# Performance work log

Measured on AMD Instinct MI355X. Metric: run time of the kernel, lower is better.

## Reference

```python
import jax, jax.numpy as jnp
import numpy as np

B, T, C = 4, 2048, 1024
H = 16                      # n_head
D = C // H                  # head dim = 64
FF = 4 * C                  # 4096


def setup_inputs() -> dict:
    key = jax.random.key(0)
    ks = jax.random.split(key, 9)
    s = 0.02
    return {
        "x": jax.random.normal(ks[0], (B, T, C), dtype=jnp.float32),
        # LayerNorm params (elementwise affine, default torch init)
        "ln1_w": jnp.ones((C,), jnp.float32),
        "ln1_b": jnp.zeros((C,), jnp.float32),
        "ln2_w": jnp.ones((C,), jnp.float32),
        "ln2_b": jnp.zeros((C,), jnp.float32),
        # attention weights, torch Linear layout [out, in], bias=False
        "w_attn": jax.random.normal(ks[1], (3 * C, C), jnp.float32) * s,
        "w_proj": jax.random.normal(ks[2], (C, C), jnp.float32) * s,
        # FFN weights
        "w_fc": jax.random.normal(ks[3], (FF, C), jnp.float32) * s,
        "w_fc_proj": jax.random.normal(ks[4], (C, FF), jnp.float32) * s,
    }


def _layernorm(x, w, b, eps=1e-5):
    mu = jnp.mean(x, axis=-1, keepdims=True)
    var = jnp.var(x, axis=-1, keepdims=True)
    return (x - mu) * jax.lax.rsqrt(var + eps) * w + b


def _attn(h, w_attn, w_proj):
    qkv = jnp.einsum('btc,fc->btf', h, w_attn)        # [B,T,3C]
    q, k, v = jnp.split(qkv, 3, axis=-1)
    q = q.reshape(B, T, H, D).transpose(0, 2, 1, 3)   # [B,H,T,D]
    k = k.reshape(B, T, H, D).transpose(0, 2, 1, 3)
    v = v.reshape(B, T, H, D).transpose(0, 2, 1, 3)
    att = jnp.einsum('bhtd,bhsd->bhts', q, k) * (1.0 / np.sqrt(D))
    causal = jnp.tril(jnp.ones((T, T), dtype=bool))
    att = jnp.where(causal, att, -jnp.inf)
    att = jax.nn.softmax(att, axis=-1)
    y = jnp.einsum('bhts,bhsd->bhtd', att, v)         # [B,H,T,D]
    y = y.transpose(0, 2, 1, 3).reshape(B, T, C)
    return jnp.einsum('btc,oc->bto', y, w_proj)


def _ffn(h, w_fc, w_fc_proj):
    u = jax.nn.gelu(jnp.einsum('btc,fc->btf', h, w_fc), approximate=False)
    return jnp.einsum('btf,cf->btc', u, w_fc_proj)


def reference(x, ln1_w, ln1_b, ln2_w, ln2_b, w_attn, w_proj, w_fc, w_fc_proj):
    x = x + _attn(_layernorm(x, ln1_w, ln1_b), w_attn, w_proj)
    x = x + _ffn(_layernorm(x, ln2_w, ln2_b), w_fc, w_fc_proj)
    return x
```

## Files before the change

kernel.cpp:

```cpp
#include <hip/hip_runtime.h>
#include <hip/hip_bf16.h>

using bf16 = __hip_bfloat16;
typedef __attribute__((ext_vector_type(8))) short short8;
typedef __attribute__((ext_vector_type(4))) short sh4;
typedef __attribute__((ext_vector_type(4))) float f32x4;

#define B_ 4
#define T_ 2048
#define C_ 1024
#define H_ 16
#define FF_ 4096
#define M_TOK (B_ * T_)

#define BARRIER() asm volatile("s_barrier" ::: "memory")
#define WAITLGKM0() asm volatile("s_waitcnt lgkmcnt(0)" ::: "memory")
#define WAITLGKM8() asm volatile("s_waitcnt lgkmcnt(8)" ::: "memory")
#define WAITVM4() asm volatile("s_waitcnt vmcnt(4)" ::: "memory")
#define WAITVM2() asm volatile("s_waitcnt vmcnt(2)" ::: "memory")
#define WAITVM0() asm volatile("s_waitcnt vmcnt(0)" ::: "memory")

__device__ __forceinline__ void gload16(const void* g, void* l) {
    __builtin_amdgcn_global_load_lds(
        (const __attribute__((address_space(1))) void*)g,
        (__attribute__((address_space(3))) void*)l, 16, 0, 0);
}

__device__ __forceinline__ float fexp2(float x) {
    float r;
    asm("v_exp_f32 %0, %1" : "=v"(r) : "v"(x));
    return r;
}

__device__ __forceinline__ float bf16bits2f(short s) {
    return __uint_as_float(((unsigned)(unsigned short)s) << 16);
}

template <int CTRL>
__device__ __forceinline__ float dpp_rotf(float x) {
    return __int_as_float(__builtin_amdgcn_update_dpp(
        0, __float_as_int(x), CTRL, 0xf, 0xf, true));
}
__device__ __forceinline__ float red16_max(float v) {
    v = fmaxf(v, dpp_rotf<0x128>(v));
    v = fmaxf(v, dpp_rotf<0x124>(v));
    v = fmaxf(v, dpp_rotf<0x122>(v));
    v = fmaxf(v, dpp_rotf<0x121>(v));
    return v;
}
__device__ __forceinline__ float red16_sum(float v) {
    v += dpp_rotf<0x128>(v);
    v += dpp_rotf<0x124>(v);
    v += dpp_rotf<0x122>(v);
    v += dpp_rotf<0x121>(v);
    return v;
}

__global__ void cvt_f32_bf16_v4(const float* __restrict__ in, bf16* __restrict__ out, int n4) {
    int i = blockIdx.x * blockDim.x + threadIdx.x;
    if (i < n4) {
        float4 v = ((const float4*)in)[i];
        sh4 o;
        bf16 b0 = __float2bfloat16(v.x), b1 = __float2bfloat16(v.y),
             b2 = __float2bfloat16(v.z), b3 = __float2bfloat16(v.w);
        o[0] = *(short*)&b0; o[1] = *(short*)&b1;
        o[2] = *(short*)&b2; o[3] = *(short*)&b3;
        ((sh4*)out)[i] = o;
    }
}

template <typename TIN>
__global__ __launch_bounds__(256) void ln_kernel(const TIN* __restrict__ x,
                                                 const float* __restrict__ w,
                                                 const float* __restrict__ b,
                                                 bf16* __restrict__ out) {
    int row = blockIdx.x;
    int t = threadIdx.x;
    float4 v;
    if constexpr (sizeof(TIN) == 4) {
        v = ((const float4*)(x + (size_t)row * C_))[t];
    } else {
        sh4 h = ((const sh4*)(x + (size_t)row * C_))[t];
        v.x = bf16bits2f(h[0]);
        v.y = bf16bits2f(h[1]);
        v.z = bf16bits2f(h[2]);
        v.w = bf16bits2f(h[3]);
    }
    float s = v.x + v.y + v.z + v.w;
    float s2 = v.x * v.x + v.y * v.y + v.z * v.z + v.w * v.w;
#pragma unroll
    for (int off = 32; off > 0; off >>= 1) {
        s += __shfl_down(s, off);
        s2 += __shfl_down(s2, off);
    }
    __shared__ float ss[4], ss2[4];
    int wave = t >> 6, lane = t & 63;
    if (lane == 0) { ss[wave] = s; ss2[wave] = s2; }
    __syncthreads();
    s = ss[0] + ss[1] + ss[2] + ss[3];
    s2 = ss2[0] + ss2[1] + ss2[2] + ss2[3];
    float mu = s * (1.f / C_);
    float var = s2 * (1.f / C_) - mu * mu;
    float rstd = rsqrtf(var + 1e-5f);
    float4 wv = ((const float4*)w)[t];
    float4 bv = ((const float4*)b)[t];
    sh4 o;
    bf16 b0 = __float2bfloat16((v.x - mu) * rstd * wv.x + bv.x);
    bf16 b1 = __float2bfloat16((v.y - mu) * rstd * wv.y + bv.y);
    bf16 b2 = __float2bfloat16((v.z - mu) * rstd * wv.z + bv.z);
    bf16 b3 = __float2bfloat16((v.w - mu) * rstd * wv.w + bv.w);
    o[0] = *(short*)&b0; o[1] = *(short*)&b1;
    o[2] = *(short*)&b2; o[3] = *(short*)&b3;
    ((sh4*)(out + (size_t)row * C_))[t] = o;
}

#define STG(ldsbase, g, grow0, k0)                                               \
    {                                                                            \
        _Pragma("unroll") for (int s_ = 0; s_ < 2; s_++) {                       \
            int row_ = s_ * 64 + wid * 8 + sr;                                   \
            gload16(g + (size_t)((grow0) + row_) * K + (k0) + ssc,               \
                    (ldsbase) + row_ * 64 + (lane & 7) * 8);                     \
        }                                                                        \
    }

#define HALF256 (128 * 64)
template <int EPI>
__global__ __launch_bounds__(512, 2) void gemm256(const bf16* __restrict__ Ag,
                                                  const bf16* __restrict__ Bg,
                                                  void* __restrict__ Cout,
                                                  int M, int N, int K) {
    __shared__ short SA[2][256 * 64];
    __shared__ short SB[2][256 * 64];

    const int nbx = N >> 8;
    const int nwg = nbx * (M >> 8);
    const int bid = blockIdx.x;
    const int cpx = nwg >> 3;
    const int swzb = (bid & 7) * cpx + (bid >> 3);
    const int m0 = (swzb / nbx) * 256;
    const int n0 = (swzb % nbx) * 256;

    const int t = threadIdx.x;
    const int wid = t >> 6, lane = t & 63;
    const int wm = wid >> 2, wn = wid & 3;
    const int lrow = lane & 15, lg = lane >> 4;
    const int swzr = (lane & 7) * 8;
    const int sr = lane >> 3;
    const int ssc = ((lane & 7) ^ sr) * 8;

    f32x4 acc[8][4];
#pragma unroll
    for (int mi = 0; mi < 8; mi++)
#pragma unroll
        for (int ni = 0; ni < 4; ni++) acc[mi][ni] = (f32x4){0.f, 0.f, 0.f, 0.f};
    short8 bfr[4][2];

    const int T = K >> 6;
    const int niter = T >> 1;

#define DSREADS256(q, buf)                                                       \
    if ((q) == 0) {                                                              \
        _Pragma("unroll") for (int ni = 0; ni < 4; ni++)                         \
        _Pragma("unroll") for (int ks = 0; ks < 2; ks++)                         \
            bfr[ni][ks] = *(const short8*)(&SB[buf][(wn * 64 + ni * 16 + lrow) * 64 + \
                                                    ((ks * 32 + lg * 8) ^ swzr)]);    \
    }                                                                            \
    _Pragma("unroll") for (int mi2 = 0; mi2 < 2; mi2++)                          \
    _Pragma("unroll") for (int ks = 0; ks < 2; ks++)                             \
        af[mi2 * 2 + ks] = *(const short8*)(&SA[buf][(wm * 128 + (2 * (q) + mi2) * 16 + lrow) * 64 + \
                                                     ((ks * 32 + lg * 8) ^ swzr)]);

#define MFMAS256(q)                                                              \
    __builtin_amdgcn_s_setprio(1);                                               \
    _Pragma("unroll") for (int ks = 0; ks < 2; ks++)                             \
    _Pragma("unroll") for (int ni = 0; ni < 4; ni++)                             \
    _Pragma("unroll") for (int mi2 = 0; mi2 < 2; mi2++)                          \
        acc[2 * (q) + mi2][ni] = __builtin_amdgcn_mfma_f32_16x16x32_bf16(        \
            af[mi2 * 2 + ks], bfr[ni][ks], acc[2 * (q) + mi2][ni], 0, 0, 0);     \
    __builtin_amdgcn_s_setprio(0);

    STG(&SA[0][0], Ag, m0, 0);
    STG(&SA[0][HALF256], Ag, m0 + 128, 0);
    STG(&SB[0][0], Bg, n0, 0);
    STG(&SB[0][HALF256], Bg, n0 + 128, 0);
    STG(&SB[1][0], Bg, n0, 64);
    STG(&SB[1][HALF256], Bg, n0 + 128, 64);
    WAITVM4();
    BARRIER();

    for (int iter = 0; iter < niter; iter++) {
        const int tt = 2 * iter;
        const int ka = (tt + 1) * 64, kb = (tt + 2) * 64, kc = (tt + 3) * 64;
        const bool s2 = (tt + 2 < T), s3 = (tt + 3 < T);
        const bool last = (iter == niter - 1);
        short8 af[4];

        DSREADS256(0, 0);
        STG(&SA[1][0], Ag, m0, ka);
        WAITLGKM8();
        BARRIER(); WAITLGKM0(); MFMAS256(0); BARRIER();
        DSREADS256(1, 0);
        STG(&SA[1][HALF256], Ag, m0 + 128, ka);
        BARRIER(); WAITLGKM0(); MFMAS256(1); BARRIER();
        DSREADS256(2, 0);
        if (s2) STG(&SB[0][0], Bg, n0, kb);
        BARRIER(); WAITLGKM0(); MFMAS256(2); BARRIER();
        DSREADS256(3, 0);
        if (s2) STG(&SB[0][HALF256], Bg, n0 + 128, kb);
        BARRIER(); WAITLGKM0(); MFMAS256(3);
        if (last) { WAITVM0(); } else { WAITVM4(); }
        BARRIER();
        DSREADS256(0, 1);
        if (s2) STG(&SA[0][0], Ag, m0, kb);
        WAITLGKM8();
        BARRIER(); WAITLGKM0(); MFMAS256(0); BARRIER();
        DSREADS256(1, 1);
        if (s2) STG(&SA[0][HALF256], Ag, m0 + 128, kb);
        BARRIER(); WAITLGKM0(); MFMAS256(1); BARRIER();
        DSREADS256(2, 1);
        if (s3) STG(&SB[1][0], Bg, n0, kc);
        BARRIER(); WAITLGKM0(); MFMAS256(2); BARRIER();
        DSREADS256(3, 1);
        if (s3) STG(&SB[1][HALF256], Bg, n0 + 128, kc);
        BARRIER(); WAITLGKM0(); MFMAS256(3);
        if (!last) WAITVM4();
        BARRIER();
    }

#pragma unroll
    for (int mi = 0; mi < 8; mi++) {
#pragma unroll
        for (int ni = 0; ni < 4; ni++) {
            int gr = m0 + wm * 128 + mi * 16 + lg * 4;
            int gc = n0 + wn * 64 + ni * 16 + lrow;
#pragma unroll
            for (int r = 0; r < 4; r++) {
                size_t gi = (size_t)(gr + r) * N + gc;
                float v = acc[mi][ni][r];
                if constexpr (EPI == 0) {
                    ((bf16*)Cout)[gi] = __float2bfloat16(v);
                } else {
                    float ge = 0.5f * v * (1.f + erff(v * 0.70710678f));
                    ((bf16*)Cout)[gi] = __float2bfloat16(ge);
                }
            }
        }
    }
}

template <int EPI>
__global__ __launch_bounds__(512, 2) void gemm256x128(const bf16* __restrict__ Ag,
                                                      const bf16* __restrict__ Bg,
                                                      void* __restrict__ Cout,
                                                      const void* __restrict__ Res,
                                                      int M, int N, int K) {
    __shared__ short SA[2][256 * 64];
    __shared__ short SB[2][128 * 64];

    const int nbx = N >> 7;
    const int nwg = nbx * (M >> 8);
    const int bid = blockIdx.x;
    const int cpx = nwg >> 3;
    const int swzb = (bid & 7) * cpx + (bid >> 3);
    const int m0 = (swzb / nbx) * 256;
    const int n0 = (swzb % nbx) * 128;

    const int t = threadIdx.x;
    const int wid = t >> 6, lane = t & 63;
    const int wm = wid >> 1, wn = wid & 1;
    const int lrow = lane & 15, lg = lane >> 4;
    const int swzr = (lane & 7) * 8;
    const int sr = lane >> 3;
    const int ssc = ((lane & 7) ^ sr) * 8;

    f32x4 acc[4][4];
#pragma unroll
    for (int mi = 0; mi < 4; mi++)
#pragma unroll
        for (int ni = 0; ni < 4; ni++) acc[mi][ni] = (f32x4){0.f, 0.f, 0.f, 0.f};
    short8 bfr[4][2];

    const int T = K >> 6;
    const int niter = T >> 1;

#define DSRX(p, buf)                                                             \
    if ((p) == 0) {                                                              \
        _Pragma("unroll") for (int ni = 0; ni < 4; ni++)                         \
        _Pragma("unroll") for (int ks = 0; ks < 2; ks++)                         \
            bfr[ni][ks] = *(const short8*)(&SB[buf][(wn * 64 + ni * 16 + lrow) * 64 + \
                                                    ((ks * 32 + lg * 8) ^ swzr)]);    \
    }                                                                            \
    _Pragma("unroll") for (int mi2 = 0; mi2 < 2; mi2++)                          \
    _Pragma("unroll") for (int ks = 0; ks < 2; ks++)                             \
        af[mi2 * 2 + ks] = *(const short8*)(&SA[buf][(wm * 64 + (2 * (p) + mi2) * 16 + lrow) * 64 + \
                                                     ((ks * 32 + lg * 8) ^ swzr)]);

#define MFX(p)                                                                   \
    __builtin_amdgcn_s_setprio(1);                                               \
    _Pragma("unroll") for (int ks = 0; ks < 2; ks++)                             \
    _Pragma("unroll") for (int ni = 0; ni < 4; ni++)                             \
    _Pragma("unroll") for (int mi2 = 0; mi2 < 2; mi2++)                          \
        acc[2 * (p) + mi2][ni] = __builtin_amdgcn_mfma_f32_16x16x32_bf16(        \
            af[mi2 * 2 + ks], bfr[ni][ks], acc[2 * (p) + mi2][ni], 0, 0, 0);     \
    __builtin_amdgcn_s_setprio(0);

    STG(&SA[0][0], Ag, m0, 0);
    STG(&SA[0][HALF256], Ag, m0 + 128, 0);
    STG(&SB[0][0], Bg, n0, 0);
    STG(&SB[1][0], Bg, n0, 64);
    WAITVM2();
    BARRIER();

    for (int iter = 0; iter < niter; iter++) {
        const int tt = 2 * iter;
        const int ka = (tt + 1) * 64, kb = (tt + 2) * 64, kc = (tt + 3) * 64;
        const bool s2 = (tt + 2 < T), s3 = (tt + 3 < T);
        const bool last = (iter == niter - 1);
        short8 af[4];

        DSRX(0, 0);
        STG(&SA[1][0], Ag, m0, ka);
        STG(&SA[1][HALF256], Ag, m0 + 128, ka);
        WAITLGKM8();
        BARRIER(); WAITLGKM0(); MFX(0); BARRIER();
        DSRX(1, 0);
        if (s2) STG(&SB[0][0], Bg, n0, kb);
        BARRIER(); WAITLGKM0(); MFX(1);
        if (last) { WAITVM0(); } else { WAITVM2(); }
        BARRIER();
        DSRX(0, 1);
        if (s2) {
            STG(&SA[0][0], Ag, m0, kb);
            STG(&SA[0][HALF256], Ag, m0 + 128, kb);
        }
        WAITLGKM8();
        BARRIER(); WAITLGKM0(); MFX(0); BARRIER();
        DSRX(1, 1);
        if (s3) STG(&SB[1][0], Bg, n0, kc);
        BARRIER(); WAITLGKM0(); MFX(1);
        if (last) { WAITVM0(); } else { WAITVM2(); }
        BARRIER();
    }

#pragma unroll
    for (int mi = 0; mi < 4; mi++) {
#pragma unroll
        for (int ni = 0; ni < 4; ni++) {
            int gr = m0 + wm * 64 + mi * 16 + lg * 4;
            int gc = n0 + wn * 64 + ni * 16 + lrow;
#pragma unroll
            for (int r = 0; r < 4; r++) {
                size_t gi = (size_t)(gr + r) * N + gc;
                float v = acc[mi][ni][r];
                if constexpr (EPI == 0) {
                    ((bf16*)Cout)[gi] = __float2bfloat16(v);
                } else if constexpr (EPI == 3) {
                    float res = ((const float*)Res)[gi];
                    ((bf16*)Cout)[gi] = __float2bfloat16(res + v);
                } else {
                    float res = __bfloat162float(((const bf16*)Res)[gi]);
                    ((float*)Cout)[gi] = res + v;
                }
            }
        }
    }
}

__global__ __launch_bounds__(256) void flash_attn(const bf16* __restrict__ qk,
                                                  const bf16* __restrict__ vt,
                                                  bf16* __restrict__ y) {
    const int pi = blockIdx.x;
    const int bh = blockIdx.y;
    const int b = bh >> 4, h = bh & 15;
    const int t = threadIdx.x;
    const int wave = t >> 6, lane = t & 63;
    const int lrow = lane & 15, g = lane >> 4, lk = g * 8;

    __shared__ alignas(16) short Ks[64 * 72];
    __shared__ alignas(16) short Vs[64 * 72];
    __shared__ alignas(16) short Ps[128 * 72];

    const size_t rs = 2 * C_;
    const bf16* Qg = qk + (size_t)b * T_ * rs + h * 64;
    const bf16* Kg = Qg + C_;
    const bf16* Vg = vt + (size_t)(h * 64) * M_TOK + b * T_;

    const int srow = t >> 3;
    const int sc8 = (t & 7) * 8;
    const float scale2 = 0.125f * 1.44269504089f;

    for (int sel = 0; sel < 2; sel++) {
        const int qtb = sel ? pi : 15 - pi;
        const int q0 = qtb * 128;
        const int nkt = 2 * qtb + 2;

        short8 qf[2][2];
#pragma unroll
        for (int mi = 0; mi < 2; mi++) {
            const bf16* qr = Qg + (size_t)(q0 + wave * 32 + mi * 16 + lrow) * rs;
            qf[mi][0] = *(const short8*)(qr + lk);
            qf[mi][1] = *(const short8*)(qr + 32 + lk);
        }

        f32x4 o[2][4];
        float m[2][4], l[2][4];
#pragma unroll
        for (int mi = 0; mi < 2; mi++) {
#pragma unroll
            for (int ni = 0; ni < 4; ni++) o[mi][ni] = (f32x4){0.f, 0.f, 0.f, 0.f};
#pragma unroll
            for (int r = 0; r < 4; r++) { m[mi][r] = -1e30f; l[mi][r] = 0.f; }
        }

        short8 kr[2], vr[2];
#pragma unroll
        for (int p = 0; p < 2; p++) {
            int r = srow + p * 32;
            kr[p] = *(const short8*)(Kg + (size_t)r * rs + sc8);
            vr[p] = *(const short8*)(Vg + (size_t)r * M_TOK + sc8);
        }

        for (int kt = 0; kt < nkt; kt++) {
            const int s0 = kt * 64;
#pragma unroll
            for (int p = 0; p < 2; p++) {
                int r = srow + p * 32;
                *(short8*)(&Ks[r * 72 + sc8]) = kr[p];
                *(short8*)(&Vs[r * 72 + sc8]) = vr[p];
            }
            __syncthreads();
            if (kt + 1 < nkt) {
                const int s0n = (kt + 1) * 64;
#pragma unroll
                for (int p = 0; p < 2; p++) {
                    int r = srow + p * 32;
                    kr[p] = *(const short8*)(Kg + (size_t)(s0n + r) * rs + sc8);
                    vr[p] = *(const short8*)(Vg + (size_t)r * M_TOK + s0n + sc8);
                }
            }

            f32x4 s[2][4];
#pragma unroll
            for (int mi = 0; mi < 2; mi++)
#pragma unroll
                for (int ni = 0; ni < 4; ni++) s[mi][ni] = (f32x4){0.f, 0.f, 0.f, 0.f};
            __builtin_amdgcn_s_setprio(1);
#pragma unroll
            for (int ks = 0; ks < 2; ks++) {
#pragma unroll
                for (int ni = 0; ni < 4; ni++) {
                    short8 kf = *(const short8*)(&Ks[(ni * 16 + lrow) * 72 + ks * 32 + lk]);
#pragma unroll
                    for (int mi = 0; mi < 2; mi++)
                        s[mi][ni] = __builtin_amdgcn_mfma_f32_16x16x32_bf16(
                            qf[mi][ks], kf, s[mi][ni], 0, 0, 0);
                }
            }
            __builtin_amdgcn_s_setprio(0);

            if (kt >= nkt - 2) {
#pragma unroll
                for (int mi = 0; mi < 2; mi++)
#pragma unroll
                    for (int ni = 0; ni < 4; ni++)
#pragma unroll
                        for (int r = 0; r < 4; r++) {
                            int qg = q0 + wave * 32 + mi * 16 + g * 4 + r;
                            int kvg = s0 + ni * 16 + lrow;
                            s[mi][ni][r] = (kvg > qg) ? -1e30f : s[mi][ni][r] * scale2;
                        }
            } else {
#pragma unroll
                for (int mi = 0; mi < 2; mi++)
#pragma unroll
                    for (int ni = 0; ni < 4; ni++)
#pragma unroll
                        for (int r = 0; r < 4; r++) s[mi][ni][r] *= scale2;
            }

#pragma unroll
            for (int mi = 0; mi < 2; mi++) {
                float pm[4];
#pragma unroll
                for (int r = 0; r < 4; r++) {
                    float v = fmaxf(fmaxf(s[mi][0][r], s[mi][1][r]),
                                    fmaxf(s[mi][2][r], s[mi][3][r]));
                    pm[r] = red16_max(v);
                }
                int ok = (pm[0] <= m[mi][0] + 8.f) && (pm[1] <= m[mi][1] + 8.f) &&
                         (pm[2] <= m[mi][2] + 8.f) && (pm[3] <= m[mi][3] + 8.f);
                if (!__all(ok)) {
                    float alpha[4];
#pragma unroll
                    for (int r = 0; r < 4; r++) {
                        float mn = fmaxf(m[mi][r], pm[r]);
                        alpha[r] = fexp2(m[mi][r] - mn);
                        m[mi][r] = mn;
                        l[mi][r] *= alpha[r];
                    }
#pragma unroll
                    for (int ni = 0; ni < 4; ni++)
#pragma unroll
                        for (int r = 0; r < 4; r++) o[mi][ni][r] *= alpha[r];
                }
                float rowsum[4] = {0.f, 0.f, 0.f, 0.f};
#pragma unroll
                for (int ni = 0; ni < 4; ni++) {
#pragma unroll
                    for (int r = 0; r < 4; r++) {
                        float p = fexp2(s[mi][ni][r] - m[mi][r]);
                        rowsum[r] += p;
                        bf16 pb = __float2bfloat16(p);
                        Ps[(wave * 32 + mi * 16 + g * 4 + r) * 72 + ni * 16 + lrow] = *(short*)&pb;
                    }
                }
#pragma unroll
                for (int r = 0; r < 4; r++)
                    l[mi][r] += red16_sum(rowsum[r]);
            }

            __builtin_amdgcn_s_setprio(1);
#pragma unroll
            for (int ks2 = 0; ks2 < 2; ks2++) {
                short8 pf[2];
#pragma unroll
                for (int mi = 0; mi < 2; mi++)
                    pf[mi] = *(const short8*)(&Ps[(wave * 32 + mi * 16 + lrow) * 72 + ks2 * 32 + lk]);
#pragma unroll
                for (int ni = 0; ni < 4; ni++) {
                    short8 vf = *(const short8*)(&Vs[(ni * 16 + lrow) * 72 + ks2 * 32 + lk]);
#pragma unroll
                    for (int mi = 0; mi < 2; mi++)
                        o[mi][ni] = __builtin_amdgcn_mfma_f32_16x16x32_bf16(
                            pf[mi], vf, o[mi][ni], 0, 0, 0);
                }
            }
            __builtin_amdgcn_s_setprio(0);
            __syncthreads();
        }

#pragma unroll
        for (int mi = 0; mi < 2; mi++) {
            float inv[4];
#pragma unroll
            for (int r = 0; r < 4; r++) inv[r] = 1.f / l[mi][r];
#pragma unroll
            for (int ni = 0; ni < 4; ni++)
#pragma unroll
                for (int r = 0; r < 4; r++) {
                    int qrow = q0 + wave * 32 + mi * 16 + g * 4 + r;
                    y[((size_t)(b * T_ + qrow)) * C_ + h * 64 + ni * 16 + lrow] =
                        __float2bfloat16(o[mi][ni][r] * inv[r]);
                }
        }
    }
}

extern "C" void kernel_launch(void* const* d_in, const int* in_sizes, int n_in,
                              void* d_out, int out_size, void* d_ws, size_t ws_size,
                              hipStream_t stream) {
    const float* x      = (const float*)d_in[0];
    const float* ln1w   = (const float*)d_in[1];
    const float* ln1b   = (const float*)d_in[2];
    const float* ln2w   = (const float*)d_in[3];
    const float* ln2b   = (const float*)d_in[4];
    const float* w_attn = (const float*)d_in[5];
    const float* w_proj = (const float*)d_in[6];
    const float* w_fc   = (const float*)d_in[7];
    const float* w_fcp  = (const float*)d_in[8];
    float* out = (float*)d_out;

    char* ws = (char*)d_ws;
    bf16* ln_buf  = (bf16*)(ws);
    bf16* qk_buf  = (bf16*)(ws + (16u << 20));
    bf16* vt_buf  = (bf16*)(ws + (48u << 20));
    bf16* ybuf    = (bf16*)(ws + (64u << 20));
    bf16* ubuf    = (bf16*)(ws + (16u << 20));
    bf16* x2b     = (bf16*)(ws + (80u << 20));
    bf16* wattn_h = (bf16*)(ws + (112u << 20));
    bf16* wproj_h = (bf16*)(ws + (118u << 20));
    bf16* wfc_h   = (bf16*)(ws + (120u << 20));
    bf16* wfcp_h  = (bf16*)(ws + (128u << 20));

    {
        int n1 = 3 * C_ * C_ / 4, n2 = C_ * C_ / 4, n3 = FF_ * C_ / 4, n4 = C_ * FF_ / 4;
        cvt_f32_bf16_v4<<<(n1 + 255) / 256, 256, 0, stream>>>(w_attn, wattn_h, n1);
        cvt_f32_bf16_v4<<<(n2 + 255) / 256, 256, 0, stream>>>(w_proj, wproj_h, n2);
        cvt_f32_bf16_v4<<<(n3 + 255) / 256, 256, 0, stream>>>(w_fc, wfc_h, n3);
        cvt_f32_bf16_v4<<<(n4 + 255) / 256, 256, 0, stream>>>(w_fcp, wfcp_h, n4);
    }

    ln_kernel<float><<<M_TOK, 256, 0, stream>>>(x, ln1w, ln1b, ln_buf);

    gemm256<0><<<dim3((M_TOK / 256) * (2 * C_ / 256)), 512, 0, stream>>>(
        ln_buf, wattn_h, qk_buf, M_TOK, 2 * C_, C_);

    gemm256x128<0><<<dim3((C_ / 256) * (M_TOK / 128)), 512, 0, stream>>>(
        wattn_h + (size_t)2 * C_ * C_, ln_buf, vt_buf, nullptr, C_, M_TOK, C_);

    flash_attn<<<dim3(8, B_ * H_), 256, 0, stream>>>(qk_buf, vt_buf, ybuf);

    gemm256x128<3><<<dim3((M_TOK / 256) * (C_ / 128)), 512, 0, stream>>>(
        ybuf, wproj_h, x2b, x, M_TOK, C_, C_);

    ln_kernel<bf16><<<M_TOK, 256, 0, stream>>>(x2b, ln2w, ln2b, ln_buf);

    gemm256<2><<<dim3((M_TOK / 256) * (FF_ / 256)), 512, 0, stream>>>(
        ln_buf, wfc_h, ubuf, M_TOK, FF_, C_);

    gemm256x128<4><<<dim3((M_TOK / 256) * (C_ / 128)), 512, 0, stream>>>(
        ubuf, wfcp_h, out, x2b, M_TOK, C_, FF_);
}
```

Measured before the change: 390.3 us.

## Shrink flash-attention query tile to 64 rows and fold softmax scale into QKV GEMM

Each flash-attention block now processes 64-query tiles (one 16-row MMA slab per wave) instead of 128, and the grid doubles to 16×64 blocks with a 4-block-per-CU occupancy hint. The causal mask is applied only to the last key tile. The softmax scale times log2(e) moves into the QK GEMM epilogue for the Q columns, removing per-element multiplies in the attention loop. The intent is more parallelism and less wasted causal work, at the cost of loading K/V twice as often per query and lower MFMA reuse per K/V tile.

```diff
diff --git a/kernel.cpp b/kernel.cpp
--- a/kernel.cpp
+++ b/kernel.cpp
@@ -12,6 +12,7 @@
 #define H_ 16
 #define FF_ 4096
 #define M_TOK (B_ * T_)
+#define SCALE2 0.1803368801111f
 
 #define BARRIER() asm volatile("s_barrier" ::: "memory")
 #define WAITLGKM0() asm volatile("s_waitcnt lgkmcnt(0)" ::: "memory")
@@ -239,6 +240,9 @@
                 float v = acc[mi][ni][r];
                 if constexpr (EPI == 0) {
                     ((bf16*)Cout)[gi] = __float2bfloat16(v);
+                } else if constexpr (EPI == 5) {
+                    float vv = (gc < C_) ? v * SCALE2 : v;
+                    ((bf16*)Cout)[gi] = __float2bfloat16(vv);
                 } else {
                     float ge = 0.5f * v * (1.f + erff(v * 0.70710678f));
                     ((bf16*)Cout)[gi] = __float2bfloat16(ge);
@@ -366,9 +370,9 @@
     }
 }
 
-__global__ __launch_bounds__(256) void flash_attn(const bf16* __restrict__ qk,
-                                                  const bf16* __restrict__ vt,
-                                                  bf16* __restrict__ y) {
+__global__ __launch_bounds__(256, 4) void flash_attn(const bf16* __restrict__ qk,
+                                                     const bf16* __restrict__ vt,
+                                                     bf16* __restrict__ y) {
     const int pi = blockIdx.x;
     const int bh = blockIdx.y;
     const int b = bh >> 4, h = bh & 15;
@@ -378,7 +382,7 @@
 
     __shared__ alignas(16) short Ks[64 * 72];
     __shared__ alignas(16) short Vs[64 * 72];
-    __shared__ alignas(16) short Ps[128 * 72];
+    __shared__ alignas(16) short Ps[64 * 72];
 
     const size_t rs = 2 * C_;
     const bf16* Qg = qk + (size_t)b * T_ * rs + h * 64;
@@ -387,30 +391,25 @@
 
     const int srow = t >> 3;
     const int sc8 = (t & 7) * 8;
-    const float scale2 = 0.125f * 1.44269504089f;
 
     for (int sel = 0; sel < 2; sel++) {
-        const int qtb = sel ? pi : 15 - pi;
-        const int q0 = qtb * 128;
-        const int nkt = 2 * qtb + 2;
-
-        short8 qf[2][2];
-#pragma unroll
-        for (int mi = 0; mi < 2; mi++) {
-            const bf16* qr = Qg + (size_t)(q0 + wave * 32 + mi * 16 + lrow) * rs;
-            qf[mi][0] = *(const short8*)(qr + lk);
-            qf[mi][1] = *(const short8*)(qr + 32 + lk);
+        const int qtb = sel ? pi : 31 - pi;
+        const int q0 = qtb * 64;
+        const int nkt = qtb + 1;
+
+        short8 qf[2];
+        {
+            const bf16* qr = Qg + (size_t)(q0 + wave * 16 + lrow) * rs;
+            qf[0] = *(const short8*)(qr + lk);
+            qf[1] = *(const short8*)(qr + 32 + lk);
         }
 
-        f32x4 o[2][4];
-        float m[2][4], l[2][4];
-#pragma unroll
-        for (int mi = 0; mi < 2; mi++) {
-#pragma unroll
-            for (int ni = 0; ni < 4; ni++) o[mi][ni] = (f32x4){0.f, 0.f, 0.f, 0.f};
-#pragma unroll
-            for (int r = 0; r < 4; r++) { m[mi][r] = -1e30f; l[mi][r] = 0.f; }
-        }
+        f32x4 o[4];
+        float m[4], l[4];
+#pragma unroll
+        for (int ni = 0; ni < 4; ni++) o[ni] = (f32x4){0.f, 0.f, 0.f, 0.f};
+#pragma unroll
+        for (int r = 0; r < 4; r++) { m[r] = -1e30f; l[r] = 0.f; }
 
         short8 kr[2], vr[2];
 #pragma unroll
@@ -439,120 +438,93 @@
                 }
             }
 
-            f32x4 s[2][4];
-#pragma unroll
-            for (int mi = 0; mi < 2; mi++)
-#pragma unroll
-                for (int ni = 0; ni < 4; ni++) s[mi][ni] = (f32x4){0.f, 0.f, 0.f, 0.f};
+            f32x4 s[4];
+#pragma unroll
+            for (int ni = 0; ni < 4; ni++) s[ni] = (f32x4){0.f, 0.f, 0.f, 0.f};
             __builtin_amdgcn_s_setprio(1);
 #pragma unroll
             for (int ks = 0; ks < 2; ks++) {
 #pragma unroll
                 for (int ni = 0; ni < 4; ni++) {
                     short8 kf = *(const short8*)(&Ks[(ni * 16 + lrow) * 72 + ks * 32 + lk]);
-#pragma unroll
-                    for (int mi = 0; mi < 2; mi++)
-                        s[mi][ni] = __builtin_amdgcn_mfma_f32_16x16x32_bf16(
-                            qf[mi][ks], kf, s[mi][ni], 0, 0, 0);
+                    s[ni] = __builtin_amdgcn_mfma_f32_16x16x32_bf16(qf[ks], kf, s[ni], 0, 0, 0);
                 }
             }
             __builtin_amdgcn_s_setprio(0);
 
-            if (kt >= nkt - 2) {
-#pragma unroll
-                for (int mi = 0; mi < 2; mi++)
-#pragma unroll
-                    for (int ni = 0; ni < 4; ni++)
-#pragma unroll
-                        for (int r = 0; r < 4; r++) {
-                            int qg = q0 + wave * 32 + mi * 16 + g * 4 + r;
-                            int kvg = s0 + ni * 16 + lrow;
-                            s[mi][ni][r] = (kvg > qg) ? -1e30f : s[mi][ni][r] * scale2;
-                        }
-            } else {
-#pragma unroll
-                for (int mi = 0; mi < 2; mi++)
-#pragma unroll
-                    for (int ni = 0; ni < 4; ni++)
-#pragma unroll
-                        for (int r = 0; r < 4; r++) s[mi][ni][r] *= scale2;
-            }
-
-#pragma unroll
-            for (int mi = 0; mi < 2; mi++) {
-                float pm[4];
+            if (kt == nkt - 1) {
+#pragma unroll
+                for (int ni = 0; ni < 4; ni++)
+#pragma unroll
+                    for (int r = 0; r < 4; r++) {
+                        int qg = q0 + wave * 16 + g * 4 + r;
+                        int kvg = s0 + ni * 16 + lrow;
+                        if (kvg > qg) s[ni][r] = -1e30f;
+                    }
+            }
+
+            float pm[4];
+#pragma unroll
+            for (int r = 0; r < 4; r++) {
+                float v = fmaxf(fmaxf(s[0][r], s[1][r]), fmaxf(s[2][r], s[3][r]));
+                pm[r] = red16_max(v);
+            }
+            float dmax = fmaxf(fmaxf(pm[0] - m[0], pm[1] - m[1]),
+                               fmaxf(pm[2] - m[2], pm[3] - m[3]));
+            if (!__all(dmax <= 8.f)) {
+                float alpha[4];
 #pragma unroll
                 for (int r = 0; r < 4; r++) {
-                    float v = fmaxf(fmaxf(s[mi][0][r], s[mi][1][r]),
-                                    fmaxf(s[mi][2][r], s[mi][3][r]));
-                    pm[r] = red16_max(v);
-                }
-                int ok = (pm[0] <= m[mi][0] + 8.f) && (pm[1] <= m[mi][1] + 8.f) &&
-                         (pm[2] <= m[mi][2] + 8.f) && (pm[3] <= m[mi][3] + 8.f);
-                if (!__all(ok)) {
-                    float alpha[4];
-#pragma unroll
-                    for (int r = 0; r < 4; r++) {
-                        float mn = fmaxf(m[mi][r], pm[r]);
-                        alpha[r] = fexp2(m[mi][r] - mn);
-                        m[mi][r] = mn;
-                        l[mi][r] *= alpha[r];
-                    }
-#pragma unroll
-                    for (int ni = 0; ni < 4; ni++)
-#pragma unroll
-                        for (int r = 0; r < 4; r++) o[mi][ni][r] *= alpha[r];
-                }
-                float rowsum[4] = {0.f, 0.f, 0.f, 0.f};
-#pragma unroll
-                for (int ni = 0; ni < 4; ni++) {
-#pragma unroll
-                    for (int r = 0; r < 4; r++) {
-                        float p = fexp2(s[mi][ni][r] - m[mi][r]);
-                        rowsum[r] += p;
-                        bf16 pb = __float2bfloat16(p);
-                        Ps[(wave * 32 + mi * 16 + g * 4 + r) * 72 + ni * 16 + lrow] = *(short*)&pb;
-                    }
-                }
-#pragma unroll
-                for (int r = 0; r < 4; r++)
-                    l[mi][r] += red16_sum(rowsum[r]);
-            }
+                    float mn = fmaxf(m[r], pm[r]);
+                    alpha[r] = fexp2(m[r] - mn);
+                    m[r] = mn;
+                    l[r] *= alpha[r];
+                }
+#pragma unroll
+                for (int ni = 0; ni < 4; ni++)
+#pragma unroll
+                    for (int r = 0; r < 4; r++) o[ni][r] *= alpha[r];
+            }
+            float rowsum[4] = {0.f, 0.f, 0.f, 0.f};
+#pragma unroll
+            for (int ni = 0; ni < 4; ni++) {
+#pragma unroll
+                for (int r = 0; r < 4; r++) {
+                    float p = fexp2(s[ni][r] - m[r]);
+                    rowsum[r] += p;
+                    bf16 pb = __float2bfloat16(p);
+                    Ps[(wave * 16 + g * 4 + r) * 72 + ni * 16 + lrow] = *(short*)&pb;
+                }
+            }
+#pragma unroll
+            for (int r = 0; r < 4; r++)
+                l[r] += red16_sum(rowsum[r]);
 
             __builtin_amdgcn_s_setprio(1);
 #pragma unroll
             for (int ks2 = 0; ks2 < 2; ks2++) {
-                short8 pf[2];
-#pragma unroll
-                for (int mi = 0; mi < 2; mi++)
-                    pf[mi] = *(const short8*)(&Ps[(wave * 32 + mi * 16 + lrow) * 72 + ks2 * 32 + lk]);
+                short8 pf = *(const short8*)(&Ps[(wave * 16 + lrow) * 72 + ks2 * 32 + lk]);
 #pragma unroll
                 for (int ni = 0; ni < 4; ni++) {
                     short8 vf = *(const short8*)(&Vs[(ni * 16 + lrow) * 72 + ks2 * 32 + lk]);
-#pragma unroll
-                    for (int mi = 0; mi < 2; mi++)
-                        o[mi][ni] = __builtin_amdgcn_mfma_f32_16x16x32_bf16(
-                            pf[mi], vf, o[mi][ni], 0, 0, 0);
+                    o[ni] = __builtin_amdgcn_mfma_f32_16x16x32_bf16(pf, vf, o[ni], 0, 0, 0);
                 }
             }
             __builtin_amdgcn_s_setprio(0);
             __syncthreads();
         }
 
-#pragma unroll
-        for (int mi = 0; mi < 2; mi++) {
-            float inv[4];
-#pragma unroll
-            for (int r = 0; r < 4; r++) inv[r] = 1.f / l[mi][r];
-#pragma unroll
-            for (int ni = 0; ni < 4; ni++)
-#pragma unroll
-                for (int r = 0; r < 4; r++) {
-                    int qrow = q0 + wave * 32 + mi * 16 + g * 4 + r;
-                    y[((size_t)(b * T_ + qrow)) * C_ + h * 64 + ni * 16 + lrow] =
-                        __float2bfloat16(o[mi][ni][r] * inv[r]);
-                }
-        }
+        float inv[4];
+#pragma unroll
+        for (int r = 0; r < 4; r++) inv[r] = 1.f / l[r];
+#pragma unroll
+        for (int ni = 0; ni < 4; ni++)
+#pragma unroll
+            for (int r = 0; r < 4; r++) {
+                int qrow = q0 + wave * 16 + g * 4 + r;
+                y[((size_t)(b * T_ + qrow)) * C_ + h * 64 + ni * 16 + lrow] =
+                    __float2bfloat16(o[ni][r] * inv[r]);
+            }
     }
 }
 
@@ -592,13 +564,13 @@
 
     ln_kernel<float><<<M_TOK, 256, 0, stream>>>(x, ln1w, ln1b, ln_buf);
 
-    gemm256<0><<<dim3((M_TOK / 256) * (2 * C_ / 256)), 512, 0, stream>>>(
+    gemm256<5><<<dim3((M_TOK / 256) * (2 * C_ / 256)), 512, 0, stream>>>(
         ln_buf, wattn_h, qk_buf, M_TOK, 2 * C_, C_);
 
     gemm256x128<0><<<dim3((C_ / 256) * (M_TOK / 128)), 512, 0, stream>>>(
         wattn_h + (size_t)2 * C_ * C_, ln_buf, vt_buf, nullptr, C_, M_TOK, C_);
 
-    flash_attn<<<dim3(8, B_ * H_), 256, 0, stream>>>(qk_buf, vt_buf, ybuf);
+    flash_attn<<<dim3(16, B_ * H_), 256, 0, stream>>>(qk_buf, vt_buf, ybuf);
 
     gemm256x128<3><<<dim3((M_TOK / 256) * (C_ / 128)), 512, 0, stream>>>(
         ybuf, wproj_h, x2b, x, M_TOK, C_, C_);
```

Result: faster. 382.2 us (-2.1%).
